# Kernel tuning notes

Hardware: AMD Instinct MI355X
Metric: run time of the kernel (lower is better)

Reference implementation:

```python
import jax, jax.numpy as jnp
import numpy as np

D_MODEL = 1024
NUM_HEADS = 16
D_K = D_MODEL // NUM_HEADS
B, S = 2, 2048


def setup_inputs() -> dict:
    key = jax.random.key(0)
    ks = jax.random.split(key, 11)
    sc = 1.0 / np.sqrt(D_MODEL)
    return {
        "Q_input": jax.random.normal(ks[0], (B, S, D_MODEL), jnp.float32),
        "K_input": jax.random.normal(ks[1], (B, S, D_MODEL), jnp.float32),
        "V_input": jax.random.normal(ks[2], (B, S, D_MODEL), jnp.float32),
        "Wq": jax.random.normal(ks[3], (D_MODEL, D_MODEL), jnp.float32) * sc,
        "bq": jax.random.normal(ks[4], (D_MODEL,), jnp.float32) * 0.01,
        "Wk": jax.random.normal(ks[5], (D_MODEL, D_MODEL), jnp.float32) * sc,
        "bk": jax.random.normal(ks[6], (D_MODEL,), jnp.float32) * 0.01,
        "Wv": jax.random.normal(ks[7], (D_MODEL, D_MODEL), jnp.float32) * sc,
        "bv": jax.random.normal(ks[8], (D_MODEL,), jnp.float32) * 0.01,
        "Wo": jax.random.normal(ks[9], (D_MODEL, D_MODEL), jnp.float32) * sc,
        "bo": jax.random.normal(ks[10], (D_MODEL,), jnp.float32) * 0.01,
    }


def reference(Q_input, K_input, V_input, Wq, bq, Wk, bk, Wv, bv, Wo, bo):
    # Linear projections (torch Linear: x @ W.T + b)
    Q = Q_input @ Wq.T + bq  # [B,S,D]
    K = K_input @ Wk.T + bk
    V = V_input @ Wv.T + bv
    # split heads -> [B,H,S,dk]
    def split(x):
        return x.reshape(B, S, NUM_HEADS, D_K).transpose(0, 2, 1, 3)
    Qh, Kh, Vh = split(Q), split(K), split(V)
    scale = 1.0 / jnp.sqrt(jnp.asarray(D_K, Qh.dtype))
    scores = jnp.einsum('bhqd,bhkd->bhqk', Qh, Kh) * scale  # [B,H,S,S]
    attn = jax.nn.softmax(scores, axis=-1)
    ctx = jnp.einsum('bhqk,bhkd->bhqd', attn, Vh)  # [B,H,S,dk]
    concat = ctx.transpose(0, 2, 1, 3).reshape(B, S, D_MODEL)
    out = concat @ Wo.T + bo  # dropout is identity in eval
    return out
```

## Files before the change

### kernel.cpp

```cpp
#include <hip/hip_runtime.h>
#include <stdint.h>

#define DM   1024
#define NH   16
#define DKH  64
#define BBATCH 2
#define SEQ  2048
#define MTOK (BBATCH*SEQ)

typedef unsigned short u16;
typedef unsigned int   u32;
typedef __attribute__((ext_vector_type(8))) short  bf16x8;
typedef __attribute__((ext_vector_type(4))) float  f32x4;

struct PtrArr11 { const void* p[11]; };
struct U16Arr11 { u16* p[11]; };

__device__ __forceinline__ float bf2f(u16 u) {
  union { unsigned int i; float f; } z; z.i = ((unsigned int)u) << 16; return z.f;
}
__device__ __forceinline__ u16 f2bf(float f) {
  union { float f; unsigned int i; } z; z.f = f;
  unsigned int i = z.i + 0x7fffu + ((z.i >> 16) & 1u);
  return (u16)(i >> 16);
}

__device__ __forceinline__ bf16x8 u4_to_bf(u32 a, u32 b, u32 c, u32 d) {
  union { u32 u[4]; bf16x8 v; } z; z.u[0] = a; z.u[1] = b; z.u[2] = c; z.u[3] = d; return z.v;
}

__device__ __forceinline__ void gld16(const void* g, void* l) {
  __builtin_amdgcn_global_load_lds(
      (const __attribute__((address_space(1))) void*)g,
      (__attribute__((address_space(3))) void*)l,
      16, 0, 0);
}

__global__ void k_detect(const unsigned int* __restrict__ w, int* __restrict__ flag) {
  const int ln = threadIdx.x & 63;
  const unsigned int word = w[ln];
  const unsigned int ex = (word >> 7) & 0xFFu;
  const int hit = (ex >= 100u && ex <= 126u) ? 1 : 0;
  unsigned long long m = __ballot(hit);
  if (ln == 0) *flag = (__popcll(m) >= 40) ? 0 : 1;
}

__global__ __launch_bounds__(256) void k_convert_all(PtrArr11 src, U16Arr11 dst,
                                                     const int* __restrict__ flag) {
  if (*flag == 0) return;
  const int b = blockIdx.x;
  int seg, base;
  if      (b <  2048) { seg = 0;  base = 0;    }
  else if (b <  4096) { seg = 1;  base = 2048; }
  else if (b <  6144) { seg = 2;  base = 4096; }
  else if (b <  6656) { seg = 3;  base = 6144; }
  else if (b == 6656) { seg = 4;  base = 6656; }
  else if (b <  7169) { seg = 5;  base = 6657; }
  else if (b == 7169) { seg = 6;  base = 7169; }
  else if (b <  7682) { seg = 7;  base = 7170; }
  else if (b == 7682) { seg = 8;  base = 7682; }
  else if (b <  8195) { seg = 9;  base = 7683; }
  else                { seg = 10; base = 8195; }
  const int n = (seg < 3) ? (MTOK * DM) : ((seg & 1) ? (DM * DM) : DM);
  const int i0 = (b - base) * 2048 + threadIdx.x * 8;
  if (i0 >= n) return;
  const float* s = (const float*)src.p[seg] + i0;
  bf16x8 o;
#pragma unroll
  for (int j = 0; j < 8; ++j) o[j] = (short)f2bf(s[j]);
  *(bf16x8*)(dst.p[seg] + i0) = o;
}

__device__ __forceinline__ void gemm_body(const u16* __restrict__ X,
                                          const u16* __restrict__ W,
                                          const u16* __restrict__ bias,
                                          void* __restrict__ out,
                                          int isf32out)
{
  __shared__ __attribute__((aligned(16))) u16 sA[128 * 32];
  __shared__ __attribute__((aligned(16))) u16 sB[128 * 32];
  const int tid = threadIdx.x;
  const int ln = tid & 63, wv = tid >> 6;
  const int wm = wv & 1, wn = wv >> 1;
  const int m0 = blockIdx.y * 128, n0 = blockIdx.x * 128;
  const int fr = ln & 15, fq = ln >> 4;
  const int srow = ln >> 2, sslot = (ln & 3) * 8;

  f32x4 acc[4][4];
#pragma unroll
  for (int i = 0; i < 4; ++i)
#pragma unroll
    for (int j = 0; j < 4; ++j) acc[i][j] = (f32x4){0.f, 0.f, 0.f, 0.f};

  const u16* pA = X + (size_t)(m0 + wv * 32 + srow) * DM + sslot;
  const u16* pB = W + (size_t)(n0 + wv * 32 + srow) * DM + sslot;
  u16* lA0 = sA + (wv * 2) * 512; u16* lA1 = sA + (wv * 2 + 1) * 512;
  u16* lB0 = sB + (wv * 2) * 512; u16* lB1 = sB + (wv * 2 + 1) * 512;

  for (int k0 = 0; k0 < DM; k0 += 32) {
    gld16(pA + k0,            lA0);
    gld16(pA + 16 * DM + k0,  lA1);
    gld16(pB + k0,            lB0);
    gld16(pB + 16 * DM + k0,  lB1);
    asm volatile("s_waitcnt vmcnt(0)" ::: "memory");
    __syncthreads();

    bf16x8 af[4], bfg[4];
#pragma unroll
    for (int t = 0; t < 4; ++t) {
      af[t]  = *(const bf16x8*)(sA + (wm * 64 + t * 16 + fr) * 32 + fq * 8);
      bfg[t] = *(const bf16x8*)(sB + (wn * 64 + t * 16 + fr) * 32 + fq * 8);
    }
#pragma unroll
    for (int i = 0; i < 4; ++i)
#pragma unroll
      for (int j = 0; j < 4; ++j)
        acc[i][j] = __builtin_amdgcn_mfma_f32_16x16x32_bf16(af[i], bfg[j], acc[i][j], 0, 0, 0);
    __syncthreads();
  }

#pragma unroll
  for (int i = 0; i < 4; ++i) {
    const int row = m0 + wm * 64 + i * 16 + fq * 4;
#pragma unroll
    for (int j = 0; j < 4; ++j) {
      const int col = n0 + wn * 64 + j * 16 + fr;
      const float bv = bf2f(bias[col]);
#pragma unroll
      for (int r = 0; r < 4; ++r) {
        const float val = acc[i][j][r] + bv;
        const size_t idx = (size_t)(row + r) * DM + col;
        if (isf32out) ((float*)out)[idx] = val;
        else          ((u16*)out)[idx]   = f2bf(val);
      }
    }
  }
}

__global__ __launch_bounds__(256, 2) void k_gemm_qkv(
    PtrArr11 orig, U16Arr11 conv, const int* __restrict__ flag,
    u16* oq, u16* ok, u16* ov)
{
  const int f = *flag;
  const int z = blockIdx.z;
  const u16* X  = f ? conv.p[z]         : (const u16*)orig.p[z];
  const u16* W  = f ? conv.p[3 + 2 * z] : (const u16*)orig.p[3 + 2 * z];
  const u16* bi = f ? conv.p[4 + 2 * z] : (const u16*)orig.p[4 + 2 * z];
  u16* o = (z == 0) ? oq : (z == 1) ? ok : ov;
  gemm_body(X, W, bi, o, 0);
}

__global__ __launch_bounds__(256, 2) void k_gemm_one(
    const u16* X, const void* Wo_o, const u16* Wo_c,
    const void* bo_o, const u16* bo_c, const int* __restrict__ flag, void* o)
{
  const int f = *flag;
  const u16* W  = f ? Wo_c : (const u16*)Wo_o;
  const u16* bi = f ? bo_c : (const u16*)bo_o;
  gemm_body(X, W, bi, o, f);
}

__global__ __launch_bounds__(256) void k_transpose(const u16* __restrict__ in,
                                                   u16* __restrict__ out)
{
  __shared__ u16 t[64][66];
  const int b = blockIdx.z;
  const int s0 = blockIdx.x * 64, d0 = blockIdx.y * 64;
  const int c = threadIdx.x & 63, r0 = threadIdx.x >> 6;
#pragma unroll
  for (int i = 0; i < 16; ++i) {
    const int r = r0 + 4 * i;
    t[r][c] = in[(size_t)(b * SEQ + s0 + r) * DM + d0 + c];
  }
  __syncthreads();
#pragma unroll
  for (int i = 0; i < 16; ++i) {
    const int r = r0 + 4 * i;
    out[(size_t)(b * DM + d0 + r) * SEQ + s0 + c] = t[c][r];
  }
}

__global__ __launch_bounds__(256, 2) void k_attn(
    const u16* __restrict__ Qp, const u16* __restrict__ Kp,
    const u16* __restrict__ Vt, u16* __restrict__ ctx)
{
  __shared__ __attribute__((aligned(16))) u16 sK[2][64 * 64];
  __shared__ __attribute__((aligned(16))) u16 sV[2][64 * 64];

  const int tid = threadIdx.x;
  const int ln = tid & 63, wv = tid >> 6;
  const int bh = blockIdx.y;
  const int b = bh >> 4, h = bh & 15;
  const int q0 = blockIdx.x * 128 + wv * 32;
  const int fr = ln & 15, fq = ln >> 4;
  const int fr7 = fr & 7;

  const int srow = ln >> 3;
  const int scol = ((ln & 7) ^ srow) * 8;
  const u16* gK0 = Kp + (size_t)(b * SEQ + wv * 16 + srow) * DM + h * DKH + scol;
  const u16* gV0 = Vt + (size_t)(b * DM + h * DKH + wv * 16 + srow) * SEQ + scol;
  u16* sKb = &sK[0][0];
  u16* sVb = &sV[0][0];

  bf16x8 qf[2][2];
#pragma unroll
  for (int qt = 0; qt < 2; ++qt)
#pragma unroll
    for (int ks = 0; ks < 2; ++ks) {
      const u16* src = Qp + (size_t)(b * SEQ + q0 + qt * 16 + fr) * DM + h * DKH + ks * 32 + fq * 8;
      bf16x8 v = *(const bf16x8*)src;
      bf16x8 w;
#pragma unroll
      for (int j = 0; j < 8; ++j) w[j] = (short)f2bf(bf2f((u16)v[j]) * 0.125f);
      qf[qt][ks] = w;
    }

  float l_a[2] = {0.f, 0.f};
  float l_b[2] = {0.f, 0.f};
  f32x4 o_acc[2][4];
#pragma unroll
  for (int qt = 0; qt < 2; ++qt)
#pragma unroll
    for (int dt = 0; dt < 4; ++dt) o_acc[qt][dt] = (f32x4){0.f, 0.f, 0.f, 0.f};

#define STAGE_KV(pp, key0)                                     \
  do {                                                         \
    u16* kd = sKb + (pp) * 4096 + wv * 1024;                   \
    u16* vd = sVb + (pp) * 4096 + wv * 1024;                   \
    gld16(gK0 + (size_t)(key0) * DM, kd);                      \
    gld16(gK0 + (size_t)((key0) + 8) * DM, kd + 512);          \
    gld16(gV0 + (key0), vd);                                   \
    gld16(gV0 + (key0) + 8 * SEQ, vd + 512);                   \
  } while (0)

  STAGE_KV(0, 0);
  asm volatile("s_waitcnt vmcnt(0)" ::: "memory");
  __syncthreads();

  int p = 0;
  for (int kb = 0; kb < SEQ / 64; ++kb) {
    if (kb + 1 < SEQ / 64) STAGE_KV(p ^ 1, (kb + 1) * 64);

    const u16* K = sKb + p * 4096;
    const u16* V = sVb + p * 4096;

    bf16x8 kf[4][2];
#pragma unroll
    for (int nt = 0; nt < 4; ++nt)
#pragma unroll
      for (int ks = 0; ks < 2; ++ks)
        kf[nt][ks] = *(const bf16x8*)(K + (nt * 16 + fr) * 64 + ((ks * 4 + fq) ^ fr7) * 8);

    u32 pw[2][2][4];
#pragma unroll
    for (int qt = 0; qt < 2; ++qt) {
      f32x4 s_acc[4];
#pragma unroll
      for (int nt = 0; nt < 4; ++nt) s_acc[nt] = (f32x4){0.f, 0.f, 0.f, 0.f};
      __builtin_amdgcn_s_setprio(1);
#pragma unroll
      for (int nt = 0; nt < 4; ++nt)
#pragma unroll
        for (int ks = 0; ks < 2; ++ks)
          s_acc[nt] = __builtin_amdgcn_mfma_f32_16x16x32_bf16(kf[nt][ks], qf[qt][ks], s_acc[nt], 0, 0, 0);
      __builtin_amdgcn_s_setprio(0);

      u32 w[4][2];
#pragma unroll
      for (int nt = 0; nt < 4; ++nt)
#pragma unroll
        for (int t = 0; t < 2; ++t) {
          const float e0 = __expf(s_acc[nt][2 * t]);
          const float e1 = __expf(s_acc[nt][2 * t + 1]);
          l_a[qt] += e0;
          l_b[qt] += e1;
          u32 wd;
          asm("v_cvt_pk_bf16_f32 %0, %1, %2" : "=v"(wd) : "v"(e0), "v"(e1));
          w[nt][t] = wd;
        }
#pragma unroll
      for (int ks = 0; ks < 2; ++ks) {
        u32 a0 = w[2 * ks][0], b0 = w[2 * ks + 1][0];
        u32 a1 = w[2 * ks][1], b1 = w[2 * ks + 1][1];
        asm("v_permlane32_swap_b32 %0, %1" : "+v"(a0), "+v"(b0));
        asm("v_permlane16_swap_b32 %0, %1" : "+v"(a0), "+v"(b0));
        asm("v_permlane32_swap_b32 %0, %1" : "+v"(a1), "+v"(b1));
        asm("v_permlane16_swap_b32 %0, %1" : "+v"(a1), "+v"(b1));
        pw[qt][ks][0] = a0; pw[qt][ks][1] = a1; pw[qt][ks][2] = b0; pw[qt][ks][3] = b1;
      }
    }

#pragma unroll
    for (int dt = 0; dt < 4; ++dt) {
      bf16x8 vf0 = *(const bf16x8*)(V + (dt * 16 + fr) * 64 + ((0 + fq) ^ fr7) * 8);
      bf16x8 vf1 = *(const bf16x8*)(V + (dt * 16 + fr) * 64 + ((4 + fq) ^ fr7) * 8);
      __builtin_amdgcn_s_setprio(1);
#pragma unroll
      for (int qt = 0; qt < 2; ++qt) {
        o_acc[qt][dt] = __builtin_amdgcn_mfma_f32_16x16x32_bf16(
            u4_to_bf(pw[qt][0][0], pw[qt][0][1], pw[qt][0][2], pw[qt][0][3]), vf0, o_acc[qt][dt], 0, 0, 0);
        o_acc[qt][dt] = __builtin_amdgcn_mfma_f32_16x16x32_bf16(
            u4_to_bf(pw[qt][1][0], pw[qt][1][1], pw[qt][1][2], pw[qt][1][3]), vf1, o_acc[qt][dt], 0, 0, 0);
      }
      __builtin_amdgcn_s_setprio(0);
    }

    asm volatile("s_waitcnt vmcnt(0)" ::: "memory");
    __syncthreads();
    p ^= 1;
  }
#undef STAGE_KV

  float iv[2][4];
#pragma unroll
  for (int qt = 0; qt < 2; ++qt) {
    float t = l_a[qt] + l_b[qt];
    t += __shfl_xor(t, 16);
    t += __shfl_xor(t, 32);
    const float rl = 1.0f / t;
#pragma unroll
    for (int rr = 0; rr < 4; ++rr) iv[qt][rr] = __shfl(rl, fq * 4 + rr);
  }
#pragma unroll
  for (int qt = 0; qt < 2; ++qt)
#pragma unroll
    for (int dt = 0; dt < 4; ++dt)
#pragma unroll
      for (int r = 0; r < 4; ++r) {
        const int qrow = q0 + qt * 16 + fq * 4 + r;
        const int col = h * DKH + dt * 16 + fr;
        ctx[(size_t)(b * SEQ + qrow) * DM + col] = f2bf(o_acc[qt][dt][r] * iv[qt][r]);
      }
}

extern "C" void kernel_launch(void* const* d_in, const int* in_sizes, int n_in,
                              void* d_out, int out_size, void* d_ws, size_t ws_size,
                              hipStream_t stream)
{
  char* ws = (char*)d_ws;
  int* flag = (int*)ws;

  const size_t TOKSZ = (size_t)MTOK * DM * sizeof(u16);
  const size_t WSZ   = (size_t)DM * DM * sizeof(u16);
  const size_t BSZ   = 4096;

  size_t off = 256;
  u16* Qc  = (u16*)(ws + off); off += TOKSZ;
  u16* Kc  = (u16*)(ws + off); off += TOKSZ;
  u16* Vc  = (u16*)(ws + off); off += TOKSZ;
  u16* Wqc = (u16*)(ws + off); off += WSZ;
  u16* Wkc = (u16*)(ws + off); off += WSZ;
  u16* Wvc = (u16*)(ws + off); off += WSZ;
  u16* Woc = (u16*)(ws + off); off += WSZ;
  u16* bqc = (u16*)(ws + off); off += BSZ;
  u16* bkc = (u16*)(ws + off); off += BSZ;
  u16* bvc = (u16*)(ws + off); off += BSZ;
  u16* boc = (u16*)(ws + off); off += BSZ;
  u16* Qp  = (u16*)(ws + off); off += TOKSZ;
  u16* Kp  = (u16*)(ws + off); off += TOKSZ;
  u16* Vp  = (u16*)(ws + off); off += TOKSZ;
  u16* Vt  = Qc;
  u16* ctx = Kc;

  PtrArr11 orig;
  for (int i = 0; i < 11; ++i) orig.p[i] = d_in[i];
  U16Arr11 conv;
  conv.p[0] = Qc;  conv.p[1] = Kc;  conv.p[2] = Vc;
  conv.p[3] = Wqc; conv.p[4] = bqc; conv.p[5] = Wkc; conv.p[6] = bkc;
  conv.p[7] = Wvc; conv.p[8] = bvc; conv.p[9] = Woc; conv.p[10] = boc;

  dim3 blk(256);

  k_detect<<<1, 64, 0, stream>>>((const unsigned int*)d_in[3], flag);
  k_convert_all<<<8196, blk, 0, stream>>>(orig, conv, flag);
  k_gemm_qkv<<<dim3(DM / 128, MTOK / 128, 3), blk, 0, stream>>>(
      orig, conv, flag, Qp, Kp, Vp);
  k_transpose<<<dim3(SEQ / 64, DM / 64, BBATCH), blk, 0, stream>>>(Vp, Vt);
  k_attn<<<dim3(SEQ / 128, BBATCH * NH), blk, 0, stream>>>(Qp, Kp, Vt, ctx);
  k_gemm_one<<<dim3(DM / 128, MTOK / 128, 1), blk, 0, stream>>>(
      ctx, d_in[9], Woc, d_in[10], boc, flag, d_out);
}
```

Baseline: 236.2 us.

## Load V fragments directly from global in attention and narrow output GEMM tile

The attention kernel stops staging V through shared memory. Each wave now loads its V fragments straight from global memory (transposed V) into registers at the start of each key block, which halves LDS use and removes the LDS reads for V. Separately, the output projection uses a new 128x64 tile GEMM body so twice as many blocks are launched, aiming to fill the GPU better (256 to 512 blocks). The trade-off is that global V loads are now exposed latency with no LDS prefetch, and the new GEMM body has no double buffering.

```diff
diff --git a/kernel.cpp b/kernel.cpp
--- a/kernel.cpp
+++ b/kernel.cpp
@@ -137,6 +137,72 @@
   }
 }
 
+__device__ __forceinline__ void gemm_body_n64(const u16* __restrict__ X,
+                                              const u16* __restrict__ W,
+                                              const u16* __restrict__ bias,
+                                              void* __restrict__ out,
+                                              int isf32out)
+{
+  __shared__ __attribute__((aligned(16))) u16 sA[128 * 32];
+  __shared__ __attribute__((aligned(16))) u16 sB[64 * 32];
+  const int tid = threadIdx.x;
+  const int ln = tid & 63, wv = tid >> 6;
+  const int wm = wv >> 1, wn = wv & 1;
+  const int m0 = blockIdx.y * 128, n0 = blockIdx.x * 64;
+  const int fr = ln & 15, fq = ln >> 4;
+  const int srow = ln >> 2, sslot = (ln & 3) * 8;
+
+  f32x4 acc[4][2];
+#pragma unroll
+  for (int i = 0; i < 4; ++i)
+#pragma unroll
+    for (int j = 0; j < 2; ++j) acc[i][j] = (f32x4){0.f, 0.f, 0.f, 0.f};
+
+  const u16* pA = X + (size_t)(m0 + wv * 32 + srow) * DM + sslot;
+  const u16* pB = W + (size_t)(n0 + wv * 16 + srow) * DM + sslot;
+  u16* lA0 = sA + (wv * 2) * 512; u16* lA1 = sA + (wv * 2 + 1) * 512;
+  u16* lB  = sB + wv * 512;
+
+  for (int k0 = 0; k0 < DM; k0 += 32) {
+    gld16(pA + k0,           lA0);
+    gld16(pA + 16 * DM + k0, lA1);
+    gld16(pB + k0,           lB);
+    asm volatile("s_waitcnt vmcnt(0)" ::: "memory");
+    __syncthreads();
+
+    bf16x8 af[4], bfg[2];
+#pragma unroll
+    for (int t = 0; t < 4; ++t)
+      af[t]  = *(const bf16x8*)(sA + (wm * 64 + t * 16 + fr) * 32 + fq * 8);
+#pragma unroll
+    for (int t = 0; t < 2; ++t)
+      bfg[t] = *(const bf16x8*)(sB + (wn * 32 + t * 16 + fr) * 32 + fq * 8);
+#pragma unroll
+    for (int i = 0; i < 4; ++i)
+#pragma unroll
+      for (int j = 0; j < 2; ++j)
+        acc[i][j] = __builtin_amdgcn_mfma_f32_16x16x32_bf16(af[i], bfg[j], acc[i][j], 0, 0, 0);
+    __syncthreads();
+  }
+
+#pragma unroll
+  for (int i = 0; i < 4; ++i) {
+    const int row = m0 + wm * 64 + i * 16 + fq * 4;
+#pragma unroll
+    for (int j = 0; j < 2; ++j) {
+      const int col = n0 + wn * 32 + j * 16 + fr;
+      const float bv = bf2f(bias[col]);
+#pragma unroll
+      for (int r = 0; r < 4; ++r) {
+        const float val = acc[i][j][r] + bv;
+        const size_t idx = (size_t)(row + r) * DM + col;
+        if (isf32out) ((float*)out)[idx] = val;
+        else          ((u16*)out)[idx]   = f2bf(val);
+      }
+    }
+  }
+}
+
 __global__ __launch_bounds__(256, 2) void k_gemm_qkv(
     PtrArr11 orig, U16Arr11 conv, const int* __restrict__ flag,
     u16* oq, u16* ok, u16* ov)
@@ -157,7 +223,7 @@
   const int f = *flag;
   const u16* W  = f ? Wo_c : (const u16*)Wo_o;
   const u16* bi = f ? bo_c : (const u16*)bo_o;
-  gemm_body(X, W, bi, o, f);
+  gemm_body_n64(X, W, bi, o, f);
 }
 
 __global__ __launch_bounds__(256) void k_transpose(const u16* __restrict__ in,
@@ -185,7 +251,6 @@
     const u16* __restrict__ Vt, u16* __restrict__ ctx)
 {
   __shared__ __attribute__((aligned(16))) u16 sK[2][64 * 64];
-  __shared__ __attribute__((aligned(16))) u16 sV[2][64 * 64];
 
   const int tid = threadIdx.x;
   const int ln = tid & 63, wv = tid >> 6;
@@ -198,9 +263,9 @@
   const int srow = ln >> 3;
   const int scol = ((ln & 7) ^ srow) * 8;
   const u16* gK0 = Kp + (size_t)(b * SEQ + wv * 16 + srow) * DM + h * DKH + scol;
-  const u16* gV0 = Vt + (size_t)(b * DM + h * DKH + wv * 16 + srow) * SEQ + scol;
   u16* sKb = &sK[0][0];
-  u16* sVb = &sV[0][0];
+
+  const u16* gVb = Vt + (size_t)(b * DM + h * DKH) * SEQ;
 
   bf16x8 qf[2][2];
 #pragma unroll
@@ -223,26 +288,31 @@
 #pragma unroll
     for (int dt = 0; dt < 4; ++dt) o_acc[qt][dt] = (f32x4){0.f, 0.f, 0.f, 0.f};
 
-#define STAGE_KV(pp, key0)                                     \
+#define STAGE_K(pp, key0)                                      \
   do {                                                         \
     u16* kd = sKb + (pp) * 4096 + wv * 1024;                   \
-    u16* vd = sVb + (pp) * 4096 + wv * 1024;                   \
     gld16(gK0 + (size_t)(key0) * DM, kd);                      \
     gld16(gK0 + (size_t)((key0) + 8) * DM, kd + 512);          \
-    gld16(gV0 + (key0), vd);                                   \
-    gld16(gV0 + (key0) + 8 * SEQ, vd + 512);                   \
   } while (0)
 
-  STAGE_KV(0, 0);
+  STAGE_K(0, 0);
   asm volatile("s_waitcnt vmcnt(0)" ::: "memory");
   __syncthreads();
 
   int p = 0;
   for (int kb = 0; kb < SEQ / 64; ++kb) {
-    if (kb + 1 < SEQ / 64) STAGE_KV(p ^ 1, (kb + 1) * 64);
+    const int key0 = kb * 64;
+
+    bf16x8 vf[4][2];
+#pragma unroll
+    for (int dt = 0; dt < 4; ++dt)
+#pragma unroll
+      for (int ks = 0; ks < 2; ++ks)
+        vf[dt][ks] = *(const bf16x8*)(gVb + (size_t)(dt * 16 + fr) * SEQ + key0 + ks * 32 + fq * 8);
+
+    if (kb + 1 < SEQ / 64) STAGE_K(p ^ 1, key0 + 64);
 
     const u16* K = sKb + p * 4096;
-    const u16* V = sVb + p * 4096;
 
     bf16x8 kf[4][2];
 #pragma unroll
@@ -292,15 +362,13 @@
 
 #pragma unroll
     for (int dt = 0; dt < 4; ++dt) {
-      bf16x8 vf0 = *(const bf16x8*)(V + (dt * 16 + fr) * 64 + ((0 + fq) ^ fr7) * 8);
-      bf16x8 vf1 = *(const bf16x8*)(V + (dt * 16 + fr) * 64 + ((4 + fq) ^ fr7) * 8);
       __builtin_amdgcn_s_setprio(1);
 #pragma unroll
       for (int qt = 0; qt < 2; ++qt) {
         o_acc[qt][dt] = __builtin_amdgcn_mfma_f32_16x16x32_bf16(
-            u4_to_bf(pw[qt][0][0], pw[qt][0][1], pw[qt][0][2], pw[qt][0][3]), vf0, o_acc[qt][dt], 0, 0, 0);
+            u4_to_bf(pw[qt][0][0], pw[qt][0][1], pw[qt][0][2], pw[qt][0][3]), vf[dt][0], o_acc[qt][dt], 0, 0, 0);
         o_acc[qt][dt] = __builtin_amdgcn_mfma_f32_16x16x32_bf16(
-            u4_to_bf(pw[qt][1][0], pw[qt][1][1], pw[qt][1][2], pw[qt][1][3]), vf1, o_acc[qt][dt], 0, 0, 0);
+            u4_to_bf(pw[qt][1][0], pw[qt][1][1], pw[qt][1][2], pw[qt][1][3]), vf[dt][1], o_acc[qt][dt], 0, 0, 0);
       }
       __builtin_amdgcn_s_setprio(0);
     }
@@ -309,7 +377,7 @@
     __syncthreads();
     p ^= 1;
   }
-#undef STAGE_KV
+#undef STAGE_K
 
   float iv[2][4];
 #pragma unroll
@@ -377,6 +445,6 @@
       orig, conv, flag, Qp, Kp, Vp);
   k_transpose<<<dim3(SEQ / 64, DM / 64, BBATCH), blk, 0, stream>>>(Vp, Vt);
   k_attn<<<dim3(SEQ / 128, BBATCH * NH), blk, 0, stream>>>(Qp, Kp, Vt, ctx);
-  k_gemm_one<<<dim3(DM / 128, MTOK / 128, 1), blk, 0, stream>>>(
+  k_gemm_one<<<dim3(DM / 64, MTOK / 128, 1), blk, 0, stream>>>(
       ctx, d_in[9], Woc, d_in[10], boc, flag, d_out);
 }
```

Result: slower. 248.4 us (+5.2%).
